# Kernel tuning notes

Hardware: AMD Instinct MI355X
Metric: run time of the kernel (lower is better)

The kernel has to match this reference:

```python
import jax, jax.numpy as jnp
import numpy as np

# sparse_shape = output_shape[1:4] + [1, 0, 0]
D, H, W = 41, 160, 160
EPS = 1e-3          # BatchNorm1d eps from functools.partial
NEG = -1e30         # -inf surrogate for masked max-pool


def _conv(x, w):
    # submanifold 3x3x3 conv, bias=False; x: [B,D,H,W,C], w: [3,3,3,Ci,Co]
    return jax.lax.conv_general_dilated(
        x, w, (1, 1, 1), 'SAME', dimension_numbers=('NDHWC', 'DHWIO', 'NDHWC'))


def _bn_relu(x, mask, g, b, m, v):
    # BatchNorm1d (eval semantics, running stats) + ReLU, restricted to active voxels
    y = (x - m) * jax.lax.rsqrt(v + EPS) * g + b
    return jnp.where(mask, jnp.maximum(y, 0.0), 0.0)


def _pool(x, mask, kernel, stride, pad):
    # SparseMaxPool3d: max over ACTIVE inputs in window; output active iff any input active
    k = (1,) + kernel + (1,)
    s = (1,) + stride + (1,)
    p = ((0, 0),) + tuple((q, q) for q in pad) + ((0, 0),)
    y = jax.lax.reduce_window(jnp.where(mask, x, NEG), NEG, jax.lax.max, k, s, p)
    m = jax.lax.reduce_window(mask, False, jnp.logical_or, k, s, p)
    return jnp.where(m, y, 0.0), m


def setup_inputs():
    key = jax.random.key(0)
    ks = jax.random.split(key, 16)
    N, Cin = 80000, 16
    vf = jax.random.normal(ks[0], (N, Cin), jnp.float32)
    b = jnp.zeros((N, 1), jnp.int32)
    z = jax.random.randint(ks[1], (N, 1), 0, D)
    yy = jax.random.randint(ks[2], (N, 1), 0, H)
    xx = jax.random.randint(ks[3], (N, 1), 0, W)
    coors = jnp.concatenate([b, z, yy, xx], axis=1)  # [N, 4] = (batch, z, y, x)
    w_in = jax.random.normal(ks[4], (3, 3, 3, Cin, 32), jnp.float32) * 0.05
    w_up = jax.random.normal(ks[5], (3, 3, 3, 32, 64), jnp.float32) * 0.05
    w_mid = jax.random.normal(ks[6], (6, 3, 3, 3, 64, 64), jnp.float32) * 0.05
    bn0_gamma = jax.random.uniform(ks[7], (32,), jnp.float32, 0.5, 1.5)
    bn0_beta = jax.random.normal(ks[8], (32,), jnp.float32) * 0.1
    bn0_mean = jax.random.normal(ks[9], (32,), jnp.float32) * 0.1
    bn0_var = jax.random.uniform(ks[10], (32,), jnp.float32, 0.5, 1.5)
    bn_gamma = jax.random.uniform(ks[11], (10, 64), jnp.float32, 0.5, 1.5)
    bn_beta = jax.random.normal(ks[12], (10, 64), jnp.float32) * 0.1
    bn_mean = jax.random.normal(ks[13], (10, 64), jnp.float32) * 0.1
    bn_var = jax.random.uniform(ks[14], (10, 64), jnp.float32, 0.5, 1.5)
    return dict(voxel_features=vf, coors=coors, batch_size=1,
                w_in=w_in, w_up=w_up, w_mid=w_mid,
                bn0_gamma=bn0_gamma, bn0_beta=bn0_beta, bn0_mean=bn0_mean, bn0_var=bn0_var,
                bn_gamma=bn_gamma, bn_beta=bn_beta, bn_mean=bn_mean, bn_var=bn_var)


def reference(voxel_features, coors, batch_size, w_in, w_up, w_mid,
              bn0_gamma, bn0_beta, bn0_mean, bn0_var,
              bn_gamma, bn_beta, bn_mean, bn_var):
    B = int(batch_size)
    Cin = voxel_features.shape[-1]
    idx = (coors[:, 0], coors[:, 1], coors[:, 2], coors[:, 3])
    # SparseConvTensor -> dense grid + active-site mask (submanifold conv only
    # produces outputs at active sites, so dense conv + mask is the same math)
    x = jnp.zeros((B, D, H, W, Cin), voxel_features.dtype).at[idx].set(voxel_features)
    mask = jnp.zeros((B, D, H, W), bool).at[idx].set(True)[..., None]
    # block 0 (indice_key subm0)
    x = _bn_relu(_conv(x, w_in), mask, bn0_gamma, bn0_beta, bn0_mean, bn0_var)
    x = _bn_relu(_conv(x, w_up), mask, bn_gamma[0], bn_beta[0], bn_mean[0], bn_var[0])
    x, mask = _pool(x, mask, (3, 3, 3), (2, 1, 1), (1, 1, 1))  # D: 41 -> 21
    x = _bn_relu(x, mask, bn_gamma[1], bn_beta[1], bn_mean[1], bn_var[1])
    # block 1 (indice_key subm1)
    for i in range(3):
        x = _bn_relu(_conv(x, w_mid[i]), mask,
                     bn_gamma[2 + i], bn_beta[2 + i], bn_mean[2 + i], bn_var[2 + i])
    x, mask = _pool(x, mask, (3, 3, 3), (2, 1, 1), (0, 1, 1))  # D: 21 -> 10
    x = _bn_relu(x, mask, bn_gamma[5], bn_beta[5], bn_mean[5], bn_var[5])
    # block 2 (indice_key subm2)
    for i in range(3):
        x = _bn_relu(_conv(x, w_mid[3 + i]), mask,
                     bn_gamma[6 + i], bn_beta[6 + i], bn_mean[6 + i], bn_var[6 + i])
    x, mask = _pool(x, mask, (3, 1, 1), (2, 1, 1), (0, 0, 0))  # D: 10 -> 4
    x = _bn_relu(x, mask, bn_gamma[9], bn_beta[9], bn_mean[9], bn_var[9])
    # .dense() -> [B,C,D',H,W] then view(B, C*D', H, W)
    x = jnp.transpose(x, (0, 4, 1, 2, 3))
    b, c, d, h, w = x.shape
    return x.reshape(b, c * d, h, w)
```

## Files before the change

kernel.cpp:

```cpp
#include <hip/hip_runtime.h>
#include <hip/hip_bf16.h>
#include <stdint.h>


#define EPS 1e-3f
constexpr int Dd = 41, Hh = 160, Ww = 160;
constexpr int D1 = 21, D2 = 10;

typedef short bf16x8 __attribute__((ext_vector_type(8)));
typedef short short8 __attribute__((ext_vector_type(8)));
typedef float f32x4  __attribute__((ext_vector_type(4)));

static __device__ __forceinline__ short f2bfs(float f) {
    __hip_bfloat16 h = __float2bfloat16(f);
    return *reinterpret_cast<short*>(&h);
}
static __device__ __forceinline__ float bfs2f(short s) {
    union { unsigned u; float f; } cv;
    cv.u = ((unsigned)(unsigned short)s) << 16;
    return cv.f;
}
static __device__ __forceinline__ short8 smax8(short8 a, short8 b) {
    short8 r;
    #pragma unroll
    for (int j = 0; j < 8; ++j) r[j] = a[j] > b[j] ? a[j] : b[j];
    return r;
}

__global__ void k_scatter_winner(const int* __restrict__ coors, int* __restrict__ map, int N) {
    int i = blockIdx.x * blockDim.x + threadIdx.x;
    if (i >= N) return;
    int z = coors[i*4+1], y = coors[i*4+2], x = coors[i*4+3];
    atomicMax(&map[(z*Hh + y)*Ww + x], i);
}

__global__ void k_conv1(const float* __restrict__ feat, const int* __restrict__ coors,
                        const int* __restrict__ map, const float* __restrict__ w,
                        const float* __restrict__ g, const float* __restrict__ b,
                        const float* __restrict__ mn, const float* __restrict__ vr,
                        float* __restrict__ y1, int N) {
    int t = blockIdx.x * blockDim.x + threadIdx.x;
    int i = t >> 5, oc = t & 31;
    if (i >= N) return;
    int z = coors[i*4+1], yy = coors[i*4+2], xx = coors[i*4+3];
    int cell = (z*Hh + yy)*Ww + xx;
    if (map[cell] != i) return;
    float acc = 0.f;
    for (int dz = 0; dz < 3; ++dz) {
        int nz = z + dz - 1; if (nz < 0 || nz >= Dd) continue;
        for (int dy = 0; dy < 3; ++dy) {
            int ny = yy + dy - 1; if (ny < 0 || ny >= Hh) continue;
            for (int dx = 0; dx < 3; ++dx) {
                int nx = xx + dx - 1; if (nx < 0 || nx >= Ww) continue;
                int j = map[(nz*Hh + ny)*Ww + nx];
                if (j < 0) continue;
                const float* f = feat + j*16;
                const float* wp = w + ((dz*3+dy)*3+dx)*(16*32) + oc;
                #pragma unroll
                for (int ic = 0; ic < 16; ++ic)
                    acc += f[ic] * wp[ic*32];
            }
        }
    }
    float s = g[oc] * rsqrtf(vr[oc] + EPS);
    y1[i*32 + oc] = fmaxf((acc - mn[oc]) * s + b[oc], 0.f);
}

__global__ void k_conv2(const float* __restrict__ y1, const int* __restrict__ coors,
                        const int* __restrict__ map, const float* __restrict__ w,
                        const float* __restrict__ g, const float* __restrict__ b,
                        const float* __restrict__ mn, const float* __restrict__ vr,
                        float* __restrict__ y2, int N) {
    int t = blockIdx.x * blockDim.x + threadIdx.x;
    int i = t >> 6, oc = t & 63;
    if (i >= N) return;
    int z = coors[i*4+1], yy = coors[i*4+2], xx = coors[i*4+3];
    int cell = (z*Hh + yy)*Ww + xx;
    if (map[cell] != i) return;
    float acc = 0.f;
    for (int dz = 0; dz < 3; ++dz) {
        int nz = z + dz - 1; if (nz < 0 || nz >= Dd) continue;
        for (int dy = 0; dy < 3; ++dy) {
            int ny = yy + dy - 1; if (ny < 0 || ny >= Hh) continue;
            for (int dx = 0; dx < 3; ++dx) {
                int nx = xx + dx - 1; if (nx < 0 || nx >= Ww) continue;
                int j = map[(nz*Hh + ny)*Ww + nx];
                if (j < 0) continue;
                const float* f = y1 + j*32;
                const float* wp = w + ((dz*3+dy)*3+dx)*(32*64) + oc;
                #pragma unroll
                for (int ic = 0; ic < 32; ++ic)
                    acc += f[ic] * wp[ic*64];
            }
        }
    }
    float s = g[oc] * rsqrtf(vr[oc] + EPS);
    y2[i*64 + oc] = fmaxf((acc - mn[oc]) * s + b[oc], 0.f);
}

__global__ void k_p1zg(const float* __restrict__ y2, const int* __restrict__ map,
                       short8* __restrict__ out) {
    int t = blockIdx.x * blockDim.x + threadIdx.x;
    if (t >= D1*Hh*Ww*8) return;
    int c8 = t & 7, vox = t >> 3;
    int x = vox % Ww, y = (vox / Ww) % Hh, zo = vox / (Ww*Hh);
    float mv[8];
    #pragma unroll
    for (int q = 0; q < 8; ++q) mv[q] = 0.f;
    bool any = false;
    for (int dz = 0; dz < 3; ++dz) {
        int zi = 2*zo + dz - 1;
        if ((unsigned)zi >= (unsigned)Dd) continue;
        int j = map[(zi*Hh + y)*Ww + x];
        if (j < 0) continue;
        any = true;
        const float4* f = reinterpret_cast<const float4*>(y2 + (size_t)j*64 + c8*8);
        float4 a = f[0], b = f[1];
        mv[0] = fmaxf(mv[0], a.x); mv[1] = fmaxf(mv[1], a.y);
        mv[2] = fmaxf(mv[2], a.z); mv[3] = fmaxf(mv[3], a.w);
        mv[4] = fmaxf(mv[4], b.x); mv[5] = fmaxf(mv[5], b.y);
        mv[6] = fmaxf(mv[6], b.z); mv[7] = fmaxf(mv[7], b.w);
    }
    short8 o;
    #pragma unroll
    for (int q = 0; q < 8; ++q) o[q] = any ? f2bfs(mv[q]) : (short)0xFF80;
    out[(size_t)vox*8 + c8] = o;
}

__global__ void k_p1y(const short8* __restrict__ in, short8* __restrict__ out) {
    int t = blockIdx.x * blockDim.x + threadIdx.x;
    if (t >= D1*Hh*Ww*8) return;
    int c8 = t & 7, vox = t >> 3;
    int x = vox % Ww, y = (vox / Ww) % Hh, zo = vox / (Ww*Hh);
    size_t base = ((size_t)zo*Hh*Ww)*8;
    short8 m = in[base + ((size_t)y*Ww + x)*8 + c8];
    if (y > 0)      m = smax8(m, in[base + ((size_t)(y-1)*Ww + x)*8 + c8]);
    if (y < Hh-1)   m = smax8(m, in[base + ((size_t)(y+1)*Ww + x)*8 + c8]);
    out[(size_t)vox*8 + c8] = m;
}

__global__ void k_p1x(const short8* __restrict__ in,
                      const float* __restrict__ g, const float* __restrict__ b,
                      const float* __restrict__ mn, const float* __restrict__ vr,
                      short8* __restrict__ out, uint8_t* __restrict__ mk) {
    int t = blockIdx.x * blockDim.x + threadIdx.x;
    if (t >= D1*Hh*Ww*8) return;
    int c8 = t & 7, vox = t >> 3;
    int x = vox % Ww;
    short8 m = in[(size_t)vox*8 + c8];
    if (x > 0)      m = smax8(m, in[(size_t)(vox-1)*8 + c8]);
    if (x < Ww-1)   m = smax8(m, in[(size_t)(vox+1)*8 + c8]);
    bool occ = m[0] >= 0;
    short8 o;
    #pragma unroll
    for (int j = 0; j < 8; ++j) {
        float v = 0.f;
        if (occ) {
            int c = c8*8 + j;
            float s = g[c] * rsqrtf(vr[c] + EPS);
            v = fmaxf(bfs2f(m[j])*s + (b[c] - mn[c]*s), 0.f);
        }
        o[j] = f2bfs(v);
    }
    out[(size_t)vox*8 + c8] = o;
    if (c8 == 0) mk[vox] = occ ? 1 : 0;
}

__global__ void k_pack_w(const float* __restrict__ w, __hip_bfloat16* __restrict__ wp, int total) {
    int idx = blockIdx.x * blockDim.x + threadIdx.x;
    if (idx >= total) return;
    int j    = idx & 7;
    int lane = (idx >> 3) & 63;
    int n    = (idx >> 9) & 3;
    int h    = (idx >> 11) & 1;
    int rest = idx >> 12;
    int t    = rest % 27;
    int L    = rest / 27;
    int ic = h*32 + (lane >> 4)*8 + j;
    int oc = n*16 + (lane & 15);
    wp[idx] = __float2bfloat16(w[((size_t)(L*27 + t)*64 + ic)*64 + oc]);
}

template<int DD>
__global__ __launch_bounds__(256) void k_conv64_mfma(
        const __hip_bfloat16* __restrict__ in, const __hip_bfloat16* __restrict__ wpL,
        const uint8_t* __restrict__ mask,
        const float* __restrict__ g, const float* __restrict__ b,
        const float* __restrict__ mn, const float* __restrict__ vr,
        __hip_bfloat16* __restrict__ out) {
    const int tid = threadIdx.x;
    const int w = tid >> 6, l = tid & 63;
    const int l15 = l & 15, kg = l >> 4;
    const int x0 = blockIdx.x * 32, yb = blockIdx.y * 8 + 2*w, z = blockIdx.z;

    f32x4 acc[4][4];
    #pragma unroll
    for (int f = 0; f < 4; ++f)
        #pragma unroll
        for (int n = 0; n < 4; ++n)
            acc[f][n] = (f32x4){0.f, 0.f, 0.f, 0.f};

    const bf16x8 az = {0,0,0,0,0,0,0,0};
    int t = 0;
    for (int kz = 0; kz < 3; ++kz) {
        const int zi = z + kz - 1;
        const bool zok = (zi >= 0) && (zi < DD);
        for (int ky = 0; ky < 3; ++ky) {
            for (int kx = 0; kx < 3; ++kx, ++t) {
                #pragma unroll
                for (int h = 0; h < 2; ++h) {
                    bf16x8 bfr[4];
                    const __hip_bfloat16* wb = wpL + (size_t)(t*2 + h)*2048 + (size_t)l*8;
                    #pragma unroll
                    for (int n = 0; n < 4; ++n)
                        bfr[n] = *reinterpret_cast<const bf16x8*>(wb + n*512);
                    bf16x8 afr[4];
                    #pragma unroll
                    for (int f = 0; f < 4; ++f) {
                        int yi = yb + (f >> 1) + ky - 1;
                        int xi = x0 + (f & 1)*16 + l15 + kx - 1;
                        bool ok = zok && (unsigned)yi < (unsigned)Hh && (unsigned)xi < (unsigned)Ww;
                        if (ok) {
                            const __hip_bfloat16* ap =
                                in + ((size_t)(zi*Hh + yi)*Ww + xi)*64 + h*32 + kg*8;
                            afr[f] = *reinterpret_cast<const bf16x8*>(ap);
                        } else {
                            afr[f] = az;
                        }
                    }
                    #pragma unroll
                    for (int f = 0; f < 4; ++f)
                        #pragma unroll
                        for (int n = 0; n < 4; ++n)
                            acc[f][n] = __builtin_amdgcn_mfma_f32_16x16x32_bf16(
                                afr[f], bfr[n], acc[f][n], 0, 0, 0);
                }
            }
        }
    }

    float sc[4], sh[4];
    #pragma unroll
    for (int n = 0; n < 4; ++n) {
        int oc = n*16 + l15;
        float s = g[oc] * rsqrtf(vr[oc] + EPS);
        sc[n] = s; sh[n] = b[oc] - mn[oc]*s;
    }
    #pragma unroll
    for (int f = 0; f < 4; ++f) {
        int yv = yb + (f >> 1);
        int xb2 = x0 + (f & 1)*16 + kg*4;
        #pragma unroll
        for (int r = 0; r < 4; ++r) {
            int vox = (z*Hh + yv)*Ww + (xb2 + r);
            bool mk = mask[vox] != 0;
            #pragma unroll
            for (int n = 0; n < 4; ++n) {
                float v = mk ? fmaxf(acc[f][n][r]*sc[n] + sh[n], 0.f) : 0.f;
                out[(size_t)vox*64 + n*16 + l15] = __float2bfloat16(v);
            }
        }
    }
}

__global__ void k_p2z(const short8* __restrict__ in, const uint8_t* __restrict__ mki,
                      short8* __restrict__ out, uint8_t* __restrict__ occ) {
    int t = blockIdx.x * blockDim.x + threadIdx.x;
    if (t >= D2*Hh*Ww*8) return;
    int c8 = t & 7, vox = t >> 3;
    int x = vox % Ww, y = (vox / Ww) % Hh, zo = vox / (Ww*Hh);
    short8 m = {0,0,0,0,0,0,0,0};
    uint8_t o = 0;
    for (int dz = 0; dz < 3; ++dz) {
        int zi = 2*zo + dz;
        int cv = (zi*Hh + y)*Ww + x;
        m = smax8(m, in[(size_t)cv*8 + c8]);
        if (c8 == 0) o |= mki[cv];
    }
    out[(size_t)vox*8 + c8] = m;
    if (c8 == 0) occ[vox] = o;
}

__global__ void k_p2y(const short8* __restrict__ in, const uint8_t* __restrict__ occi,
                      short8* __restrict__ out, uint8_t* __restrict__ occ) {
    int t = blockIdx.x * blockDim.x + threadIdx.x;
    if (t >= D2*Hh*Ww*8) return;
    int c8 = t & 7, vox = t >> 3;
    int x = vox % Ww, y = (vox / Ww) % Hh, zo = vox / (Ww*Hh);
    size_t base = (size_t)zo*Hh*Ww;
    short8 m = in[(base + (size_t)y*Ww + x)*8 + c8];
    uint8_t o = (c8 == 0) ? occi[base + (size_t)y*Ww + x] : 0;
    if (y > 0) {
        m = smax8(m, in[(base + (size_t)(y-1)*Ww + x)*8 + c8]);
        if (c8 == 0) o |= occi[base + (size_t)(y-1)*Ww + x];
    }
    if (y < Hh-1) {
        m = smax8(m, in[(base + (size_t)(y+1)*Ww + x)*8 + c8]);
        if (c8 == 0) o |= occi[base + (size_t)(y+1)*Ww + x];
    }
    out[(size_t)vox*8 + c8] = m;
    if (c8 == 0) occ[vox] = o;
}

__global__ void k_p2x(const short8* __restrict__ in, const uint8_t* __restrict__ occi,
                      const float* __restrict__ g, const float* __restrict__ b,
                      const float* __restrict__ mn, const float* __restrict__ vr,
                      short8* __restrict__ out, uint8_t* __restrict__ mk) {
    int t = blockIdx.x * blockDim.x + threadIdx.x;
    if (t >= D2*Hh*Ww*8) return;
    int c8 = t & 7, vox = t >> 3;
    int x = vox % Ww;
    short8 m = in[(size_t)vox*8 + c8];
    uint8_t occ = occi[vox];
    if (x > 0)    { m = smax8(m, in[(size_t)(vox-1)*8 + c8]); occ |= occi[vox-1]; }
    if (x < Ww-1) { m = smax8(m, in[(size_t)(vox+1)*8 + c8]); occ |= occi[vox+1]; }
    short8 o;
    #pragma unroll
    for (int j = 0; j < 8; ++j) {
        float v = 0.f;
        if (occ) {
            int c = c8*8 + j;
            float s = g[c] * rsqrtf(vr[c] + EPS);
            v = fmaxf(bfs2f(m[j])*s + (b[c] - mn[c]*s), 0.f);
        }
        o[j] = f2bfs(v);
    }
    out[(size_t)vox*8 + c8] = o;
    if (c8 == 0) mk[vox] = occ ? 1 : 0;
}

__global__ __launch_bounds__(256) void k_pool3t(
        const short8* __restrict__ in, const uint8_t* __restrict__ mki,
        const float* __restrict__ g, const float* __restrict__ b,
        const float* __restrict__ mn, const float* __restrict__ vr,
        float* __restrict__ out) {
    __shared__ float lds[32][65];
    const int tid = threadIdx.x;
    const int x0 = blockIdx.x * 32, y = blockIdx.y, zo = blockIdx.z;
    {
        int xq = tid >> 3, c8 = tid & 7;
        int x = x0 + xq;
        short8 m = {0,0,0,0,0,0,0,0};
        bool occ = false;
        for (int dz = 0; dz < 3; ++dz) {
            int zi = 2*zo + dz;
            int cv = (zi*Hh + y)*Ww + x;
            m = smax8(m, in[(size_t)cv*8 + c8]);
            occ = occ || (mki[cv] != 0);
        }
        #pragma unroll
        for (int j = 0; j < 8; ++j) {
            float v = 0.f;
            if (occ) {
                int c = c8*8 + j;
                float s = g[c] * rsqrtf(vr[c] + EPS);
                v = fmaxf(bfs2f(m[j])*s + (b[c] - mn[c]*s), 0.f);
            }
            lds[xq][c8*8 + j] = v;
        }
    }
    __syncthreads();
    {
        int c = tid >> 2, xo = (tid & 3) * 8;
        size_t row = ((size_t)(c*4 + zo)*Hh + y)*Ww + x0 + xo;
        #pragma unroll
        for (int j = 0; j < 8; ++j)
            out[row + j] = lds[xo + j][c];
    }
}

extern "C" void kernel_launch(void* const* d_in, const int* in_sizes, int n_in,
                              void* d_out, int out_size, void* d_ws, size_t ws_size,
                              hipStream_t stream) {
    const float* vf    = (const float*)d_in[0];
    const int*   coors = (const int*)  d_in[1];
    const float* w_in  = (const float*)d_in[3];
    const float* w_up  = (const float*)d_in[4];
    const float* w_mid = (const float*)d_in[5];
    const float* bn0_g = (const float*)d_in[6];
    const float* bn0_b = (const float*)d_in[7];
    const float* bn0_m = (const float*)d_in[8];
    const float* bn0_v = (const float*)d_in[9];
    const float* bn_g  = (const float*)d_in[10];
    const float* bn_b  = (const float*)d_in[11];
    const float* bn_m  = (const float*)d_in[12];
    const float* bn_v  = (const float*)d_in[13];
    const int N = in_sizes[0] / 16;

    char* ws = (char*)d_ws;
    size_t off = 0;
    auto alloc = [&](size_t bytes) {
        void* p = ws + off;
        off = (off + bytes + 255) & ~(size_t)255;
        return p;
    };
    int*            map  = (int*)            alloc((size_t)Dd*Hh*Ww*4);
    float*          y1   = (float*)          alloc((size_t)N*32*4);
    float*          y2   = (float*)          alloc((size_t)N*64*4);
    uint8_t*        mk1  = (uint8_t*)        alloc((size_t)D1*Hh*Ww);
    uint8_t*        mk2  = (uint8_t*)        alloc((size_t)D2*Hh*Ww);
    uint8_t*        occa = (uint8_t*)        alloc((size_t)D2*Hh*Ww);
    uint8_t*        occb = (uint8_t*)        alloc((size_t)D2*Hh*Ww);
    __hip_bfloat16* wp   = (__hip_bfloat16*) alloc((size_t)6*27*2*4*64*8*2);
    short8*         A    = (short8*)         alloc((size_t)D1*Hh*Ww*64*2);
    short8*         B    = (short8*)         alloc((size_t)D1*Hh*Ww*64*2);
    const size_t D2G = (size_t)D2*Hh*Ww*64*2;
    short8* p2a = A;
    short8* p2b = (short8*)((char*)A + D2G);
    short8* Bq  = B;
    short8* Aq  = A;

    const int PACK_TOTAL = 6*27*2*4*64*8;
    const size_t WPL = (size_t)27*2*4*64*8;
    const int P1T = D1*Hh*Ww*8, P2T = D2*Hh*Ww*8;

    hipMemsetAsync(map, 0xFF, (size_t)Dd*Hh*Ww*4, stream);
    k_pack_w<<<(PACK_TOTAL + 255)/256, 256, 0, stream>>>(w_mid, wp, PACK_TOTAL);
    k_scatter_winner<<<(N + 255)/256, 256, 0, stream>>>(coors, map, N);
    k_conv1<<<(N*32 + 255)/256, 256, 0, stream>>>(vf, coors, map, w_in,
            bn0_g, bn0_b, bn0_m, bn0_v, y1, N);
    k_conv2<<<(N*64 + 255)/256, 256, 0, stream>>>(y1, coors, map, w_up,
            bn_g, bn_b, bn_m, bn_v, y2, N);

    k_p1zg<<<(P1T + 255)/256, 256, 0, stream>>>(y2, map, A);
    k_p1y <<<(P1T + 255)/256, 256, 0, stream>>>(A, B);
    k_p1x <<<(P1T + 255)/256, 256, 0, stream>>>(B,
            bn_g + 64, bn_b + 64, bn_m + 64, bn_v + 64, A, mk1);

    dim3 g1(Ww/32, Hh/8, D1);
    k_conv64_mfma<D1><<<g1, 256, 0, stream>>>((const __hip_bfloat16*)A, wp + 0*WPL, mk1,
            bn_g + 2*64, bn_b + 2*64, bn_m + 2*64, bn_v + 2*64, (__hip_bfloat16*)B);
    k_conv64_mfma<D1><<<g1, 256, 0, stream>>>((const __hip_bfloat16*)B, wp + 1*WPL, mk1,
            bn_g + 3*64, bn_b + 3*64, bn_m + 3*64, bn_v + 3*64, (__hip_bfloat16*)A);
    k_conv64_mfma<D1><<<g1, 256, 0, stream>>>((const __hip_bfloat16*)A, wp + 2*WPL, mk1,
            bn_g + 4*64, bn_b + 4*64, bn_m + 4*64, bn_v + 4*64, (__hip_bfloat16*)B);

    k_p2z<<<(P2T + 255)/256, 256, 0, stream>>>(B, mk1, p2a, occa);
    k_p2y<<<(P2T + 255)/256, 256, 0, stream>>>(p2a, occa, p2b, occb);
    k_p2x<<<(P2T + 255)/256, 256, 0, stream>>>(p2b, occb,
            bn_g + 5*64, bn_b + 5*64, bn_m + 5*64, bn_v + 5*64, Bq, mk2);

    dim3 g2(Ww/32, Hh/8, D2);
    k_conv64_mfma<D2><<<g2, 256, 0, stream>>>((const __hip_bfloat16*)Bq, wp + 3*WPL, mk2,
            bn_g + 6*64, bn_b + 6*64, bn_m + 6*64, bn_v + 6*64, (__hip_bfloat16*)Aq);
    k_conv64_mfma<D2><<<g2, 256, 0, stream>>>((const __hip_bfloat16*)Aq, wp + 4*WPL, mk2,
            bn_g + 7*64, bn_b + 7*64, bn_m + 7*64, bn_v + 7*64, (__hip_bfloat16*)Bq);
    k_conv64_mfma<D2><<<g2, 256, 0, stream>>>((const __hip_bfloat16*)Bq, wp + 5*WPL, mk2,
            bn_g + 8*64, bn_b + 8*64, bn_m + 8*64, bn_v + 8*64, (__hip_bfloat16*)Aq);

    dim3 g3(Ww/32, Hh, 4);
    k_pool3t<<<g3, 256, 0, stream>>>(Aq, mk2,
            bn_g + 9*64, bn_b + 9*64, bn_m + 9*64, bn_v + 9*64, (float*)d_out);
}
```

Before: 1.856 ms.

## Stage conv input halo tile in LDS with XOR swizzle per z-slice

The 64-channel MFMA conv kernel now cooperatively loads a 10x34 halo tile of one input z-slice into shared memory, using an XOR swizzle to avoid bank conflicts. The 9 in-plane taps then read A fragments from LDS instead of issuing a global load per tap, which removes the redundant global/L2 traffic for overlapping windows. It also skips out-of-range z slices entirely, fully unrolls the ky/kx loops, and requests 3 blocks per SM via launch_bounds. The cost is two barriers per z-slice plus about 43KB of LDS per block, which could limit occupancy.

```diff
diff --git a/kernel.cpp b/kernel.cpp
--- a/kernel.cpp
+++ b/kernel.cpp
@@ -182,16 +182,18 @@
 }
 
 template<int DD>
-__global__ __launch_bounds__(256) void k_conv64_mfma(
+__global__ __launch_bounds__(256, 3) void k_conv64_mfma(
         const __hip_bfloat16* __restrict__ in, const __hip_bfloat16* __restrict__ wpL,
         const uint8_t* __restrict__ mask,
         const float* __restrict__ g, const float* __restrict__ b,
         const float* __restrict__ mn, const float* __restrict__ vr,
         __hip_bfloat16* __restrict__ out) {
+    __shared__ short8 sA[10*34*8];
     const int tid = threadIdx.x;
     const int w = tid >> 6, l = tid & 63;
     const int l15 = l & 15, kg = l >> 4;
-    const int x0 = blockIdx.x * 32, yb = blockIdx.y * 8 + 2*w, z = blockIdx.z;
+    const int x0 = blockIdx.x * 32, y0 = blockIdx.y * 8, z = blockIdx.z;
+    const int yb = y0 + 2*w;
 
     f32x4 acc[4][4];
     #pragma unroll
@@ -200,13 +202,26 @@
         for (int n = 0; n < 4; ++n)
             acc[f][n] = (f32x4){0.f, 0.f, 0.f, 0.f};
 
-    const bf16x8 az = {0,0,0,0,0,0,0,0};
-    int t = 0;
     for (int kz = 0; kz < 3; ++kz) {
         const int zi = z + kz - 1;
-        const bool zok = (zi >= 0) && (zi < DD);
+        if (zi < 0 || zi >= DD) continue;
+        __syncthreads();
+        for (int c = tid; c < 2720; c += 256) {
+            int v = c >> 3, s = c & 7;
+            int ly = v / 34, lx = v - ly*34;
+            int gy = y0 - 1 + ly, gx = x0 - 1 + lx;
+            bf16x8 val = {0,0,0,0,0,0,0,0};
+            if ((unsigned)gy < (unsigned)Hh && (unsigned)gx < (unsigned)Ww)
+                val = *reinterpret_cast<const bf16x8*>(
+                        in + ((size_t)(zi*Hh + gy)*Ww + gx)*64 + s*8);
+            sA[v*8 + (s ^ (lx & 7))] = val;
+        }
+        __syncthreads();
+        #pragma unroll
         for (int ky = 0; ky < 3; ++ky) {
-            for (int kx = 0; kx < 3; ++kx, ++t) {
+            #pragma unroll
+            for (int kx = 0; kx < 3; ++kx) {
+                const int t = (kz*3 + ky)*3 + kx;
                 #pragma unroll
                 for (int h = 0; h < 2; ++h) {
                     bf16x8 bfr[4];
@@ -217,16 +232,9 @@
                     bf16x8 afr[4];
                     #pragma unroll
                     for (int f = 0; f < 4; ++f) {
-                        int yi = yb + (f >> 1) + ky - 1;
-                        int xi = x0 + (f & 1)*16 + l15 + kx - 1;
-                        bool ok = zok && (unsigned)yi < (unsigned)Hh && (unsigned)xi < (unsigned)Ww;
-                        if (ok) {
-                            const __hip_bfloat16* ap =
-                                in + ((size_t)(zi*Hh + yi)*Ww + xi)*64 + h*32 + kg*8;
-                            afr[f] = *reinterpret_cast<const bf16x8*>(ap);
-                        } else {
-                            afr[f] = az;
-                        }
+                        int ly = 2*w + (f >> 1) + ky;
+                        int lx = (f & 1)*16 + l15 + kx;
+                        afr[f] = sA[(ly*34 + lx)*8 + ((h*4 + kg) ^ (lx & 7))];
                     }
                     #pragma unroll
                     for (int f = 0; f < 4; ++f)
```

Result: faster. 1.504 ms (-19.0%).
